# Kernel optimization log

Hardware: AMD Instinct MI355X
Metric: run time of the kernel (lower is better)

Reference implementation:

```python
import jax, jax.numpy as jnp
import numpy as np

N, E = 100000, 1600000
NODE_DIM, EDGE_DIM, HID = 128, 64, 128

def _mlp(x, w1, b1, w2, b2):
    # 2-layer MLP: Linear -> ReLU -> Linear (weights stored torch-style [out,in])
    return jax.nn.relu(x @ w1.T + b1) @ w2.T + b2

def setup_inputs() -> dict:
    key = jax.random.key(0)
    ks = jax.random.split(key, 24)
    g = lambda k, shp, fan: jax.random.normal(k, shp, jnp.float32) * (1.0 / np.sqrt(fan))
    return {
        "x": jax.random.normal(ks[0], (N, NODE_DIM), jnp.float32),
        "pos": jax.random.normal(ks[1], (N, 3), jnp.float32),
        "edge_index": jax.random.randint(ks[2], (2, E), 0, N),
        "edge_attr": jax.random.normal(ks[3], (E, EDGE_DIM), jnp.float32),
        # node_net: MLP(node_dim -> hid -> hid)
        "node_w1": g(ks[4], (HID, NODE_DIM), NODE_DIM), "node_b1": jnp.zeros((HID,), jnp.float32),
        "node_w2": g(ks[5], (HID, HID), HID), "node_b2": jnp.zeros((HID,), jnp.float32),
        # edge_net: MLP(edge_dim -> hid -> hid)
        "edge_w1": g(ks[6], (HID, EDGE_DIM), EDGE_DIM), "edge_b1": jnp.zeros((HID,), jnp.float32),
        "edge_w2": g(ks[7], (HID, HID), HID), "edge_b2": jnp.zeros((HID,), jnp.float32),
        # msg_net: Linear(hid, hid)
        "msg_w": g(ks[8], (HID, HID), HID), "msg_b": jnp.zeros((HID,), jnp.float32),
        # gate: MLP(edge_dim + node_dim -> hid -> hid)
        "gate_w1": g(ks[9], (HID, EDGE_DIM + NODE_DIM), EDGE_DIM + NODE_DIM), "gate_b1": jnp.zeros((HID,), jnp.float32),
        "gate_w2": g(ks[10], (HID, HID), HID), "gate_b2": jnp.zeros((HID,), jnp.float32),
        # centroid_lin: Linear(node_dim, hid)
        "cent_w": g(ks[11], (HID, NODE_DIM), NODE_DIM), "cent_b": jnp.zeros((HID,), jnp.float32),
        # layer norm
        "ln_g": jnp.ones((HID,), jnp.float32), "ln_b": jnp.zeros((HID,), jnp.float32),
        # out_transform: Linear(hid, node_dim)
        "out_w": g(ks[12], (NODE_DIM, HID), HID), "out_b": jnp.zeros((NODE_DIM,), jnp.float32),
    }

def reference(x, pos, edge_index, edge_attr,
              node_w1, node_b1, node_w2, node_b2,
              edge_w1, edge_b1, edge_w2, edge_b2,
              msg_w, msg_b,
              gate_w1, gate_b1, gate_w2, gate_b2,
              cent_w, cent_b, ln_g, ln_b, out_w, out_b):
    row, col = edge_index[0], edge_index[1]
    h_node = _mlp(x, node_w1, node_b1, node_w2, node_b2)          # (N, HID)
    h_edge = _mlp(edge_attr, edge_w1, edge_b1, edge_w2, edge_b2)   # (E, HID)
    msg_j = (h_edge * h_node[col]) @ msg_w.T + msg_b               # (E, HID)
    gate = _mlp(jnp.concatenate([edge_attr, x[col]], axis=-1),
                gate_w1, gate_b1, gate_w2, gate_b2)                # (E, HID)
    msg_j = msg_j * jax.nn.sigmoid(gate)
    aggr = jax.ops.segment_sum(msg_j, row, num_segments=x.shape[0])  # (N, HID)
    out = (x @ cent_w.T + cent_b) + aggr
    mu = jnp.mean(out, axis=-1, keepdims=True)
    var = jnp.var(out, axis=-1, keepdims=True)
    out = (out - mu) * jax.lax.rsqrt(var + 1e-5) * ln_g + ln_b
    return jax.nn.relu(out) @ out_w.T + out_b                      # (N, NODE_DIM)
```

## Files before the change

### kernel.cpp

```cpp
#include <hip/hip_runtime.h>

#define NN 100000
#define NE 1600000

typedef __bf16 bf16;
typedef bf16 bf16x8 __attribute__((ext_vector_type(8)));
typedef bf16 bf16x4 __attribute__((ext_vector_type(4)));
typedef float f32x4 __attribute__((ext_vector_type(4)));

__device__ __forceinline__ f32x4 mfma16(bf16x8 a, bf16x8 b, f32x4 c) {
    return __builtin_amdgcn_mfma_f32_16x16x32_bf16(a, b, c, 0, 0, 0);
}

__global__ void cvt_kernel(const float* __restrict__ s, bf16* __restrict__ d, int n4) {
    int i = blockIdx.x * 256 + threadIdx.x;
    if (i < n4) {
        f32x4 v = ((const f32x4*)s)[i];
        bf16x4 o;
        o[0] = (bf16)v[0]; o[1] = (bf16)v[1]; o[2] = (bf16)v[2]; o[3] = (bf16)v[3];
        ((bf16x4*)d)[i] = o;
    }
}

__launch_bounds__(256, 3)
__global__ void node_kernel(const bf16* __restrict__ xb,
                            const bf16* __restrict__ w1, const float* __restrict__ b1,
                            const bf16* __restrict__ w2, const float* __restrict__ b2,
                            const bf16* __restrict__ wc, const float* __restrict__ bc,
                            const bf16* __restrict__ wg1,
                            bf16* __restrict__ h_node, float* __restrict__ cent,
                            float* __restrict__ gx) {
    const int S = 136;
    __shared__ __align__(16) bf16 sX[64 * S];
    __shared__ __align__(16) bf16 sH[64 * S];
    const int tid = threadIdx.x;
    const int m0 = blockIdx.x * 64;
    {
        int e = tid >> 2, p = tid & 3;
        int gm = m0 + e;
        uint4 z = {0, 0, 0, 0};
        uint4* dst = (uint4*)(sX + e * S + p * 32);
        if (gm < NN) {
            const uint4* src = (const uint4*)(xb + (size_t)gm * 128 + p * 32);
#pragma unroll
            for (int j = 0; j < 4; ++j) dst[j] = src[j];
        } else {
#pragma unroll
            for (int j = 0; j < 4; ++j) dst[j] = z;
        }
    }
    __syncthreads();
    const int lane = tid & 63, wave = tid >> 6, t16 = lane & 15, quad = lane >> 4;
    const int n0 = wave * 32, koff = quad * 8;
    const f32x4 z4 = {0.f, 0.f, 0.f, 0.f};
    f32x4 acc[4][2];

#pragma unroll
    for (int mt = 0; mt < 4; ++mt) { acc[mt][0] = z4; acc[mt][1] = z4; }
#pragma unroll
    for (int ks = 0; ks < 4; ++ks) {
        bf16x8 bb0 = *(const bf16x8*)(w1 + (n0 + t16) * 128 + ks * 32 + koff);
        bf16x8 bb1 = *(const bf16x8*)(w1 + (n0 + 16 + t16) * 128 + ks * 32 + koff);
#pragma unroll
        for (int mt = 0; mt < 4; ++mt) {
            bf16x8 a = *(const bf16x8*)(sX + (mt * 16 + t16) * S + ks * 32 + koff);
            acc[mt][0] = mfma16(a, bb0, acc[mt][0]);
            acc[mt][1] = mfma16(a, bb1, acc[mt][1]);
        }
    }
    {
        float bi0 = b1[n0 + t16], bi1 = b1[n0 + 16 + t16];
#pragma unroll
        for (int mt = 0; mt < 4; ++mt)
#pragma unroll
            for (int nt = 0; nt < 2; ++nt) {
                int n = n0 + nt * 16 + t16;
                float bb = nt ? bi1 : bi0;
#pragma unroll
                for (int r = 0; r < 4; ++r) {
                    float v = acc[mt][nt][r] + bb;
                    sH[(mt * 16 + quad * 4 + r) * S + n] = (bf16)(v > 0.f ? v : 0.f);
                }
            }
    }
    __syncthreads();

#pragma unroll
    for (int mt = 0; mt < 4; ++mt) { acc[mt][0] = z4; acc[mt][1] = z4; }
#pragma unroll
    for (int ks = 0; ks < 4; ++ks) {
        bf16x8 bb0 = *(const bf16x8*)(w2 + (n0 + t16) * 128 + ks * 32 + koff);
        bf16x8 bb1 = *(const bf16x8*)(w2 + (n0 + 16 + t16) * 128 + ks * 32 + koff);
#pragma unroll
        for (int mt = 0; mt < 4; ++mt) {
            bf16x8 a = *(const bf16x8*)(sH + (mt * 16 + t16) * S + ks * 32 + koff);
            acc[mt][0] = mfma16(a, bb0, acc[mt][0]);
            acc[mt][1] = mfma16(a, bb1, acc[mt][1]);
        }
    }
    {
        float bi0 = b2[n0 + t16], bi1 = b2[n0 + 16 + t16];
#pragma unroll
        for (int mt = 0; mt < 4; ++mt)
#pragma unroll
            for (int nt = 0; nt < 2; ++nt) {
                int n = n0 + nt * 16 + t16;
                float bb = nt ? bi1 : bi0;
#pragma unroll
                for (int r = 0; r < 4; ++r) {
                    int gm = m0 + mt * 16 + quad * 4 + r;
                    if (gm < NN) h_node[(size_t)gm * 128 + n] = (bf16)(acc[mt][nt][r] + bb);
                }
            }
    }

#pragma unroll
    for (int mt = 0; mt < 4; ++mt) { acc[mt][0] = z4; acc[mt][1] = z4; }
#pragma unroll
    for (int ks = 0; ks < 4; ++ks) {
        bf16x8 bb0 = *(const bf16x8*)(wc + (n0 + t16) * 128 + ks * 32 + koff);
        bf16x8 bb1 = *(const bf16x8*)(wc + (n0 + 16 + t16) * 128 + ks * 32 + koff);
#pragma unroll
        for (int mt = 0; mt < 4; ++mt) {
            bf16x8 a = *(const bf16x8*)(sX + (mt * 16 + t16) * S + ks * 32 + koff);
            acc[mt][0] = mfma16(a, bb0, acc[mt][0]);
            acc[mt][1] = mfma16(a, bb1, acc[mt][1]);
        }
    }
    {
        float bi0 = bc[n0 + t16], bi1 = bc[n0 + 16 + t16];
#pragma unroll
        for (int mt = 0; mt < 4; ++mt)
#pragma unroll
            for (int nt = 0; nt < 2; ++nt) {
                int n = n0 + nt * 16 + t16;
                float bb = nt ? bi1 : bi0;
#pragma unroll
                for (int r = 0; r < 4; ++r) {
                    int gm = m0 + mt * 16 + quad * 4 + r;
                    if (gm < NN) cent[(size_t)gm * 128 + n] = acc[mt][nt][r] + bb;
                }
            }
    }

#pragma unroll
    for (int mt = 0; mt < 4; ++mt) { acc[mt][0] = z4; acc[mt][1] = z4; }
#pragma unroll
    for (int ks = 0; ks < 4; ++ks) {
        bf16x8 bb0 = *(const bf16x8*)(wg1 + (n0 + t16) * 192 + 64 + ks * 32 + koff);
        bf16x8 bb1 = *(const bf16x8*)(wg1 + (n0 + 16 + t16) * 192 + 64 + ks * 32 + koff);
#pragma unroll
        for (int mt = 0; mt < 4; ++mt) {
            bf16x8 a = *(const bf16x8*)(sX + (mt * 16 + t16) * S + ks * 32 + koff);
            acc[mt][0] = mfma16(a, bb0, acc[mt][0]);
            acc[mt][1] = mfma16(a, bb1, acc[mt][1]);
        }
    }
#pragma unroll
    for (int mt = 0; mt < 4; ++mt)
#pragma unroll
        for (int nt = 0; nt < 2; ++nt) {
            int n = n0 + nt * 16 + t16;
#pragma unroll
            for (int r = 0; r < 4; ++r) {
                int gm = m0 + mt * 16 + quad * 4 + r;
                if (gm < NN) gx[(size_t)gm * 128 + n] = acc[mt][nt][r];
            }
        }
}

__launch_bounds__(256, 3)
__global__ void edge_kernel(const float* __restrict__ edge_attr,
                            const int* __restrict__ erow, const int* __restrict__ ecol,
                            const bf16* __restrict__ hnode, const float* __restrict__ gx,
                            const bf16* __restrict__ we1, const float* __restrict__ be1,
                            const bf16* __restrict__ we2, const float* __restrict__ be2,
                            const bf16* __restrict__ wm, const float* __restrict__ bm,
                            const bf16* __restrict__ wg1, const float* __restrict__ bg1,
                            const bf16* __restrict__ wg2, const float* __restrict__ bg2,
                            float* __restrict__ aggr) {
    const int SE = 72, S = 136;
    __shared__ __align__(16) bf16 sEA[64 * SE];
    __shared__ __align__(16) bf16 sX[64 * S];
    __shared__ __align__(16) bf16 sT[64 * S];
    __shared__ int rowS[64], colS[64];
    const int tid = threadIdx.x;
    const int e0 = blockIdx.x * 64;
    if (tid < 64) { rowS[tid] = erow[e0 + tid]; colS[tid] = ecol[e0 + tid]; }
    __syncthreads();
#pragma unroll
    for (int i = 0; i < 4; ++i) {
        int idx = tid * 4 + i * 1024;
        int e = idx >> 6, k = idx & 63;
        f32x4 v = *(const f32x4*)(edge_attr + (size_t)(e0 + e) * 64 + k);
        bf16x4 o;
        o[0] = (bf16)v[0]; o[1] = (bf16)v[1]; o[2] = (bf16)v[2]; o[3] = (bf16)v[3];
        *(bf16x4*)(sEA + e * SE + k) = o;
    }
    {
        int e = tid >> 2, p = tid & 3;
        const uint4* src = (const uint4*)(hnode + (size_t)colS[e] * 128 + p * 32);
        uint4* dst = (uint4*)(sX + e * S + p * 32);
#pragma unroll
        for (int j = 0; j < 4; ++j) dst[j] = src[j];
    }
    __syncthreads();
    const int lane = tid & 63, wave = tid >> 6, t16 = lane & 15, quad = lane >> 4;
    const int n0 = wave * 32, koff = quad * 8;
    const f32x4 z4 = {0.f, 0.f, 0.f, 0.f};
    f32x4 acc[4][2];

    float gval[4][2][4];
#pragma unroll
    for (int mt = 0; mt < 4; ++mt)
#pragma unroll
        for (int r = 0; r < 4; ++r) {
            const float* grow = gx + (size_t)colS[mt * 16 + quad * 4 + r] * 128;
            gval[mt][0][r] = grow[n0 + t16];
            gval[mt][1][r] = grow[n0 + 16 + t16];
        }
#pragma unroll
    for (int mt = 0; mt < 4; ++mt) { acc[mt][0] = z4; acc[mt][1] = z4; }
#pragma unroll
    for (int ks = 0; ks < 2; ++ks) {
        bf16x8 bb0 = *(const bf16x8*)(wg1 + (n0 + t16) * 192 + ks * 32 + koff);
        bf16x8 bb1 = *(const bf16x8*)(wg1 + (n0 + 16 + t16) * 192 + ks * 32 + koff);
#pragma unroll
        for (int mt = 0; mt < 4; ++mt) {
            bf16x8 a = *(const bf16x8*)(sEA + (mt * 16 + t16) * SE + ks * 32 + koff);
            acc[mt][0] = mfma16(a, bb0, acc[mt][0]);
            acc[mt][1] = mfma16(a, bb1, acc[mt][1]);
        }
    }
    {
        float bi0 = bg1[n0 + t16], bi1 = bg1[n0 + 16 + t16];
#pragma unroll
        for (int mt = 0; mt < 4; ++mt)
#pragma unroll
            for (int nt = 0; nt < 2; ++nt) {
                int n = n0 + nt * 16 + t16;
                float bb = nt ? bi1 : bi0;
#pragma unroll
                for (int r = 0; r < 4; ++r) {
                    float v = acc[mt][nt][r] + bb + gval[mt][nt][r];
                    sT[(mt * 16 + quad * 4 + r) * S + n] = (bf16)(v > 0.f ? v : 0.f);
                }
            }
    }
    __syncthreads();

    f32x4 gsig[4][2];
#pragma unroll
    for (int mt = 0; mt < 4; ++mt) { gsig[mt][0] = z4; gsig[mt][1] = z4; acc[mt][0] = z4; acc[mt][1] = z4; }
#pragma unroll
    for (int ks = 0; ks < 4; ++ks) {
        bf16x8 bb0 = *(const bf16x8*)(wg2 + (n0 + t16) * 128 + ks * 32 + koff);
        bf16x8 bb1 = *(const bf16x8*)(wg2 + (n0 + 16 + t16) * 128 + ks * 32 + koff);
#pragma unroll
        for (int mt = 0; mt < 4; ++mt) {
            bf16x8 a = *(const bf16x8*)(sT + (mt * 16 + t16) * S + ks * 32 + koff);
            gsig[mt][0] = mfma16(a, bb0, gsig[mt][0]);
            gsig[mt][1] = mfma16(a, bb1, gsig[mt][1]);
        }
    }
#pragma unroll
    for (int ks = 0; ks < 2; ++ks) {
        bf16x8 bb0 = *(const bf16x8*)(we1 + (n0 + t16) * 64 + ks * 32 + koff);
        bf16x8 bb1 = *(const bf16x8*)(we1 + (n0 + 16 + t16) * 64 + ks * 32 + koff);
#pragma unroll
        for (int mt = 0; mt < 4; ++mt) {
            bf16x8 a = *(const bf16x8*)(sEA + (mt * 16 + t16) * SE + ks * 32 + koff);
            acc[mt][0] = mfma16(a, bb0, acc[mt][0]);
            acc[mt][1] = mfma16(a, bb1, acc[mt][1]);
        }
    }
    __syncthreads();
    {
        float bi0 = bg2[n0 + t16], bi1 = bg2[n0 + 16 + t16];
#pragma unroll
        for (int mt = 0; mt < 4; ++mt)
#pragma unroll
            for (int nt = 0; nt < 2; ++nt) {
                float bb = nt ? bi1 : bi0;
#pragma unroll
                for (int r = 0; r < 4; ++r) {
                    float v = gsig[mt][nt][r] + bb;
                    gsig[mt][nt][r] = 1.f / (1.f + __expf(-v));
                }
            }
    }
    {
        float bi0 = be1[n0 + t16], bi1 = be1[n0 + 16 + t16];
#pragma unroll
        for (int mt = 0; mt < 4; ++mt)
#pragma unroll
            for (int nt = 0; nt < 2; ++nt) {
                int n = n0 + nt * 16 + t16;
                float bb = nt ? bi1 : bi0;
#pragma unroll
                for (int r = 0; r < 4; ++r) {
                    float v = acc[mt][nt][r] + bb;
                    sT[(mt * 16 + quad * 4 + r) * S + n] = (bf16)(v > 0.f ? v : 0.f);
                }
            }
    }
    __syncthreads();

#pragma unroll
    for (int mt = 0; mt < 4; ++mt) { acc[mt][0] = z4; acc[mt][1] = z4; }
#pragma unroll
    for (int ks = 0; ks < 4; ++ks) {
        bf16x8 bb0 = *(const bf16x8*)(we2 + (n0 + t16) * 128 + ks * 32 + koff);
        bf16x8 bb1 = *(const bf16x8*)(we2 + (n0 + 16 + t16) * 128 + ks * 32 + koff);
#pragma unroll
        for (int mt = 0; mt < 4; ++mt) {
            bf16x8 a = *(const bf16x8*)(sT + (mt * 16 + t16) * S + ks * 32 + koff);
            acc[mt][0] = mfma16(a, bb0, acc[mt][0]);
            acc[mt][1] = mfma16(a, bb1, acc[mt][1]);
        }
    }
    {
        float bi0 = be2[n0 + t16], bi1 = be2[n0 + 16 + t16];
#pragma unroll
        for (int mt = 0; mt < 4; ++mt)
#pragma unroll
            for (int nt = 0; nt < 2; ++nt) {
                int n = n0 + nt * 16 + t16;
                float bb = nt ? bi1 : bi0;
#pragma unroll
                for (int r = 0; r < 4; ++r) {
                    float v = acc[mt][nt][r] + bb;
                    float hv = (float)sX[(mt * 16 + quad * 4 + r) * S + n];
                    acc[mt][nt][r] = v * hv;
                }
            }
    }
    __syncthreads();
#pragma unroll
    for (int mt = 0; mt < 4; ++mt)
#pragma unroll
        for (int nt = 0; nt < 2; ++nt) {
            int n = n0 + nt * 16 + t16;
#pragma unroll
            for (int r = 0; r < 4; ++r) {
                float p = acc[mt][nt][r];
                bf16 hi = (bf16)p;
                sT[(mt * 16 + quad * 4 + r) * S + n] = hi;
                sX[(mt * 16 + quad * 4 + r) * S + n] = (bf16)(p - (float)hi);
            }
        }
    __syncthreads();

#pragma unroll
    for (int mt = 0; mt < 4; ++mt) { acc[mt][0] = z4; acc[mt][1] = z4; }
#pragma unroll
    for (int ks = 0; ks < 4; ++ks) {
        bf16x8 bb0 = *(const bf16x8*)(wm + (n0 + t16) * 128 + ks * 32 + koff);
        bf16x8 bb1 = *(const bf16x8*)(wm + (n0 + 16 + t16) * 128 + ks * 32 + koff);
#pragma unroll
        for (int mt = 0; mt < 4; ++mt) {
            bf16x8 a = *(const bf16x8*)(sT + (mt * 16 + t16) * S + ks * 32 + koff);
            acc[mt][0] = mfma16(a, bb0, acc[mt][0]);
            acc[mt][1] = mfma16(a, bb1, acc[mt][1]);
        }
    }
#pragma unroll
    for (int ks = 0; ks < 4; ++ks) {
        bf16x8 bb0 = *(const bf16x8*)(wm + (n0 + t16) * 128 + ks * 32 + koff);
        bf16x8 bb1 = *(const bf16x8*)(wm + (n0 + 16 + t16) * 128 + ks * 32 + koff);
#pragma unroll
        for (int mt = 0; mt < 4; ++mt) {
            bf16x8 a = *(const bf16x8*)(sX + (mt * 16 + t16) * S + ks * 32 + koff);
            acc[mt][0] = mfma16(a, bb0, acc[mt][0]);
            acc[mt][1] = mfma16(a, bb1, acc[mt][1]);
        }
    }
    {
        float bi0 = bm[n0 + t16], bi1 = bm[n0 + 16 + t16];
#pragma unroll
        for (int mt = 0; mt < 4; ++mt)
#pragma unroll
            for (int nt = 0; nt < 2; ++nt) {
                int n = n0 + nt * 16 + t16;
                float bb = nt ? bi1 : bi0;
#pragma unroll
                for (int r = 0; r < 4; ++r) {
                    int mloc = mt * 16 + quad * 4 + r;
                    float v = (acc[mt][nt][r] + bb) * gsig[mt][nt][r];
                    atomicAdd(aggr + (size_t)rowS[mloc] * 128 + n, v);
                }
            }
    }
}

__launch_bounds__(256, 3)
__global__ void final_kernel(const float* __restrict__ cent, const float* __restrict__ aggr,
                             const float* __restrict__ lng, const float* __restrict__ lnb,
                             const bf16* __restrict__ wo, const float* __restrict__ bo,
                             float* __restrict__ out) {
    const int S = 136;
    __shared__ __align__(16) bf16 sA[128 * S];
    const int tid = threadIdx.x;
    const int m0 = blockIdx.x * 128;
    {
        int r = tid >> 1, h = tid & 1;
        int gm = m0 + r;
        f32x4 vb[16];
        float sum = 0.f, sq = 0.f;
        if (gm < NN) {
            const f32x4* c4 = (const f32x4*)(cent + (size_t)gm * 128 + h * 64);
            const f32x4* a4 = (const f32x4*)(aggr + (size_t)gm * 128 + h * 64);
#pragma unroll
            for (int j = 0; j < 16; ++j) {
                f32x4 v = c4[j] + a4[j];
                vb[j] = v;
                sum += v[0] + v[1] + v[2] + v[3];
                sq += v[0] * v[0] + v[1] * v[1] + v[2] * v[2] + v[3] * v[3];
            }
        } else {
            f32x4 z = {0.f, 0.f, 0.f, 0.f};
#pragma unroll
            for (int j = 0; j < 16; ++j) vb[j] = z;
        }
        sum += __shfl_xor(sum, 1);
        sq += __shfl_xor(sq, 1);
        float mu = sum * (1.f / 128.f);
        float var = sq * (1.f / 128.f) - mu * mu;
        float rs = rsqrtf(var + 1e-5f);
#pragma unroll
        for (int j = 0; j < 16; ++j) {
            bf16x4 o;
#pragma unroll
            for (int c = 0; c < 4; ++c) {
                int k = h * 64 + j * 4 + c;
                float y = (vb[j][c] - mu) * rs * lng[k] + lnb[k];
                y = y > 0.f ? y : 0.f;
                o[c] = (bf16)(gm < NN ? y : 0.f);
            }
            *(bf16x4*)(sA + r * S + h * 64 + j * 4) = o;
        }
    }
    __syncthreads();
    const int lane = tid & 63, wave = tid >> 6, t16 = lane & 15, quad = lane >> 4;
    const int n0 = wave * 32, koff = quad * 8;
    const f32x4 z4 = {0.f, 0.f, 0.f, 0.f};
    f32x4 acc[8][2];
#pragma unroll
    for (int mt = 0; mt < 8; ++mt) { acc[mt][0] = z4; acc[mt][1] = z4; }
#pragma unroll
    for (int ks = 0; ks < 4; ++ks) {
        bf16x8 bb0 = *(const bf16x8*)(wo + (n0 + t16) * 128 + ks * 32 + koff);
        bf16x8 bb1 = *(const bf16x8*)(wo + (n0 + 16 + t16) * 128 + ks * 32 + koff);
#pragma unroll
        for (int mt = 0; mt < 8; ++mt) {
            bf16x8 a = *(const bf16x8*)(sA + (mt * 16 + t16) * S + ks * 32 + koff);
            acc[mt][0] = mfma16(a, bb0, acc[mt][0]);
            acc[mt][1] = mfma16(a, bb1, acc[mt][1]);
        }
    }
    {
        float bi0 = bo[n0 + t16], bi1 = bo[n0 + 16 + t16];
#pragma unroll
        for (int mt = 0; mt < 8; ++mt)
#pragma unroll
            for (int nt = 0; nt < 2; ++nt) {
                int n = n0 + nt * 16 + t16;
                float bb = nt ? bi1 : bi0;
#pragma unroll
                for (int r = 0; r < 4; ++r) {
                    int gm = m0 + mt * 16 + quad * 4 + r;
                    if (gm < NN) out[(size_t)gm * 128 + n] = acc[mt][nt][r] + bb;
                }
            }
    }
}

extern "C" void kernel_launch(void* const* d_in, const int* in_sizes, int n_in,
                              void* d_out, int out_size, void* d_ws, size_t ws_size,
                              hipStream_t stream) {
    bf16* wsb = (bf16*)d_ws;
    bf16* nw1 = wsb + 0;
    bf16* nw2 = wsb + 16384;
    bf16* cw = wsb + 32768;
    bf16* ew1 = wsb + 49152;
    bf16* ew2 = wsb + 57344;
    bf16* mw = wsb + 73728;
    bf16* gw1 = wsb + 90112;
    bf16* gw2 = wsb + 114688;
    bf16* ow = wsb + 131072;
    bf16* xb = wsb + 147456;
    bf16* hb = xb + (size_t)NN * 128;
    float* cent = (float*)(hb + (size_t)NN * 128);
    float* aggr = cent + (size_t)NN * 128;
    float* gx = aggr + (size_t)NN * 128;

    auto cv = [&](int idx, bf16* dst, int n) {
        cvt_kernel<<<(n / 4 + 255) / 256, 256, 0, stream>>>((const float*)d_in[idx], dst, n / 4);
    };
    cv(4, nw1, 16384);
    cv(6, nw2, 16384);
    cv(18, cw, 16384);
    cv(8, ew1, 8192);
    cv(10, ew2, 16384);
    cv(12, mw, 16384);
    cv(14, gw1, 24576);
    cv(16, gw2, 16384);
    cv(22, ow, 16384);
    cv(0, xb, NN * 128);
    hipMemsetAsync(aggr, 0, (size_t)NN * 128 * sizeof(float), stream);

    node_kernel<<<(NN + 63) / 64, 256, 0, stream>>>(
        xb, nw1, (const float*)d_in[5], nw2, (const float*)d_in[7],
        cw, (const float*)d_in[19], gw1, hb, cent, gx);

    const int* ei = (const int*)d_in[2];
    edge_kernel<<<NE / 64, 256, 0, stream>>>(
        (const float*)d_in[3], ei, ei + NE, hb, gx,
        ew1, (const float*)d_in[9], ew2, (const float*)d_in[11],
        mw, (const float*)d_in[13], gw1, (const float*)d_in[15],
        gw2, (const float*)d_in[17], aggr);

    final_kernel<<<(NN + 127) / 128, 256, 0, stream>>>(
        cent, aggr, (const float*)d_in[20], (const float*)d_in[21],
        ow, (const float*)d_in[23], (float*)d_out);
}
```

Baseline: 1.402 ms.

## Restructure edge kernel so each wave owns 16 edges with all output columns

The edge kernel now gives each wave its own 16 edges and computes all 128 output columns per wave. Previously four waves split the columns of a shared 64-edge tile, which needed block-wide syncs, so this removes every __syncthreads and gives each wave private LDS tiles. h_node is now stored in fp32 and gathered straight into registers instead of staged in LDS as bf16, and s_setprio is raised around the MFMA loops. In exchange, weight fragments are reloaded per wave from global/L1 with less reuse across the 16-row tile, h_node gather traffic doubles, and register pressure rises.

```diff
diff --git a/kernel.cpp b/kernel.cpp
--- a/kernel.cpp
+++ b/kernel.cpp
@@ -28,7 +28,7 @@
                             const bf16* __restrict__ w2, const float* __restrict__ b2,
                             const bf16* __restrict__ wc, const float* __restrict__ bc,
                             const bf16* __restrict__ wg1,
-                            bf16* __restrict__ h_node, float* __restrict__ cent,
+                            float* __restrict__ h_node, float* __restrict__ cent,
                             float* __restrict__ gx) {
     const int S = 136;
     __shared__ __align__(16) bf16 sX[64 * S];
@@ -109,7 +109,7 @@
 #pragma unroll
                 for (int r = 0; r < 4; ++r) {
                     int gm = m0 + mt * 16 + quad * 4 + r;
-                    if (gm < NN) h_node[(size_t)gm * 128 + n] = (bf16)(acc[mt][nt][r] + bb);
+                    if (gm < NN) h_node[(size_t)gm * 128 + n] = acc[mt][nt][r] + bb;
                 }
             }
     }
@@ -172,7 +172,7 @@
 __launch_bounds__(256, 3)
 __global__ void edge_kernel(const float* __restrict__ edge_attr,
                             const int* __restrict__ erow, const int* __restrict__ ecol,
-                            const bf16* __restrict__ hnode, const float* __restrict__ gx,
+                            const float* __restrict__ hnode, const float* __restrict__ gx,
                             const bf16* __restrict__ we1, const float* __restrict__ be1,
                             const bf16* __restrict__ we2, const float* __restrict__ be2,
                             const bf16* __restrict__ wm, const float* __restrict__ bm,
@@ -180,216 +180,179 @@
                             const bf16* __restrict__ wg2, const float* __restrict__ bg2,
                             float* __restrict__ aggr) {
     const int SE = 72, S = 136;
-    __shared__ __align__(16) bf16 sEA[64 * SE];
-    __shared__ __align__(16) bf16 sX[64 * S];
-    __shared__ __align__(16) bf16 sT[64 * S];
-    __shared__ int rowS[64], colS[64];
+    __shared__ __align__(16) bf16 sEA[4][16 * SE];
+    __shared__ __align__(16) bf16 sT[4][16 * S];
+    __shared__ __align__(16) bf16 sL[4][16 * S];
     const int tid = threadIdx.x;
-    const int e0 = blockIdx.x * 64;
-    if (tid < 64) { rowS[tid] = erow[e0 + tid]; colS[tid] = ecol[e0 + tid]; }
-    __syncthreads();
-#pragma unroll
-    for (int i = 0; i < 4; ++i) {
-        int idx = tid * 4 + i * 1024;
-        int e = idx >> 6, k = idx & 63;
-        f32x4 v = *(const f32x4*)(edge_attr + (size_t)(e0 + e) * 64 + k);
-        bf16x4 o;
-        o[0] = (bf16)v[0]; o[1] = (bf16)v[1]; o[2] = (bf16)v[2]; o[3] = (bf16)v[3];
-        *(bf16x4*)(sEA + e * SE + k) = o;
-    }
-    {
-        int e = tid >> 2, p = tid & 3;
-        const uint4* src = (const uint4*)(hnode + (size_t)colS[e] * 128 + p * 32);
-        uint4* dst = (uint4*)(sX + e * S + p * 32);
-#pragma unroll
-        for (int j = 0; j < 4; ++j) dst[j] = src[j];
-    }
-    __syncthreads();
-    const int lane = tid & 63, wave = tid >> 6, t16 = lane & 15, quad = lane >> 4;
-    const int n0 = wave * 32, koff = quad * 8;
+    const int wave = tid >> 6, lane = tid & 63, t16 = lane & 15, quad = lane >> 4;
+    const int koff = quad * 8;
+    const int e0w = blockIdx.x * 64 + wave * 16;
+    bf16* sEAw = sEA[wave];
+    bf16* sTw = sT[wave];
+    bf16* sLw = sL[wave];
     const f32x4 z4 = {0.f, 0.f, 0.f, 0.f};
-    f32x4 acc[4][2];
-
-    float gval[4][2][4];
-#pragma unroll
-    for (int mt = 0; mt < 4; ++mt)
-#pragma unroll
-        for (int r = 0; r < 4; ++r) {
-            const float* grow = gx + (size_t)colS[mt * 16 + quad * 4 + r] * 128;
-            gval[mt][0][r] = grow[n0 + t16];
-            gval[mt][1][r] = grow[n0 + 16 + t16];
-        }
-#pragma unroll
-    for (int mt = 0; mt < 4; ++mt) { acc[mt][0] = z4; acc[mt][1] = z4; }
-#pragma unroll
-    for (int ks = 0; ks < 2; ++ks) {
-        bf16x8 bb0 = *(const bf16x8*)(wg1 + (n0 + t16) * 192 + ks * 32 + koff);
-        bf16x8 bb1 = *(const bf16x8*)(wg1 + (n0 + 16 + t16) * 192 + ks * 32 + koff);
-#pragma unroll
-        for (int mt = 0; mt < 4; ++mt) {
-            bf16x8 a = *(const bf16x8*)(sEA + (mt * 16 + t16) * SE + ks * 32 + koff);
-            acc[mt][0] = mfma16(a, bb0, acc[mt][0]);
-            acc[mt][1] = mfma16(a, bb1, acc[mt][1]);
-        }
-    }
-    {
-        float bi0 = bg1[n0 + t16], bi1 = bg1[n0 + 16 + t16];
-#pragma unroll
-        for (int mt = 0; mt < 4; ++mt)
-#pragma unroll
-            for (int nt = 0; nt < 2; ++nt) {
-                int n = n0 + nt * 16 + t16;
-                float bb = nt ? bi1 : bi0;
-#pragma unroll
-                for (int r = 0; r < 4; ++r) {
-                    float v = acc[mt][nt][r] + bb + gval[mt][nt][r];
-                    sT[(mt * 16 + quad * 4 + r) * S + n] = (bf16)(v > 0.f ? v : 0.f);
-                }
-            }
-    }
-    __syncthreads();
-
-    f32x4 gsig[4][2];
-#pragma unroll
-    for (int mt = 0; mt < 4; ++mt) { gsig[mt][0] = z4; gsig[mt][1] = z4; acc[mt][0] = z4; acc[mt][1] = z4; }
-#pragma unroll
-    for (int ks = 0; ks < 4; ++ks) {
-        bf16x8 bb0 = *(const bf16x8*)(wg2 + (n0 + t16) * 128 + ks * 32 + koff);
-        bf16x8 bb1 = *(const bf16x8*)(wg2 + (n0 + 16 + t16) * 128 + ks * 32 + koff);
-#pragma unroll
-        for (int mt = 0; mt < 4; ++mt) {
-            bf16x8 a = *(const bf16x8*)(sT + (mt * 16 + t16) * S + ks * 32 + koff);
-            gsig[mt][0] = mfma16(a, bb0, gsig[mt][0]);
-            gsig[mt][1] = mfma16(a, bb1, gsig[mt][1]);
-        }
-    }
-#pragma unroll
-    for (int ks = 0; ks < 2; ++ks) {
-        bf16x8 bb0 = *(const bf16x8*)(we1 + (n0 + t16) * 64 + ks * 32 + koff);
-        bf16x8 bb1 = *(const bf16x8*)(we1 + (n0 + 16 + t16) * 64 + ks * 32 + koff);
-#pragma unroll
-        for (int mt = 0; mt < 4; ++mt) {
-            bf16x8 a = *(const bf16x8*)(sEA + (mt * 16 + t16) * SE + ks * 32 + koff);
-            acc[mt][0] = mfma16(a, bb0, acc[mt][0]);
-            acc[mt][1] = mfma16(a, bb1, acc[mt][1]);
-        }
-    }
-    __syncthreads();
-    {
-        float bi0 = bg2[n0 + t16], bi1 = bg2[n0 + 16 + t16];
-#pragma unroll
-        for (int mt = 0; mt < 4; ++mt)
-#pragma unroll
-            for (int nt = 0; nt < 2; ++nt) {
-                float bb = nt ? bi1 : bi0;
-#pragma unroll
-                for (int r = 0; r < 4; ++r) {
-                    float v = gsig[mt][nt][r] + bb;
-                    gsig[mt][nt][r] = 1.f / (1.f + __expf(-v));
-                }
-            }
-    }
-    {
-        float bi0 = be1[n0 + t16], bi1 = be1[n0 + 16 + t16];
-#pragma unroll
-        for (int mt = 0; mt < 4; ++mt)
-#pragma unroll
-            for (int nt = 0; nt < 2; ++nt) {
-                int n = n0 + nt * 16 + t16;
-                float bb = nt ? bi1 : bi0;
-#pragma unroll
-                for (int r = 0; r < 4; ++r) {
-                    float v = acc[mt][nt][r] + bb;
-                    sT[(mt * 16 + quad * 4 + r) * S + n] = (bf16)(v > 0.f ? v : 0.f);
-                }
-            }
-    }
-    __syncthreads();
-
-#pragma unroll
-    for (int mt = 0; mt < 4; ++mt) { acc[mt][0] = z4; acc[mt][1] = z4; }
-#pragma unroll
-    for (int ks = 0; ks < 4; ++ks) {
-        bf16x8 bb0 = *(const bf16x8*)(we2 + (n0 + t16) * 128 + ks * 32 + koff);
-        bf16x8 bb1 = *(const bf16x8*)(we2 + (n0 + 16 + t16) * 128 + ks * 32 + koff);
-#pragma unroll
-        for (int mt = 0; mt < 4; ++mt) {
-            bf16x8 a = *(const bf16x8*)(sT + (mt * 16 + t16) * S + ks * 32 + koff);
-            acc[mt][0] = mfma16(a, bb0, acc[mt][0]);
-            acc[mt][1] = mfma16(a, bb1, acc[mt][1]);
-        }
-    }
-    {
-        float bi0 = be2[n0 + t16], bi1 = be2[n0 + 16 + t16];
-#pragma unroll
-        for (int mt = 0; mt < 4; ++mt)
-#pragma unroll
-            for (int nt = 0; nt < 2; ++nt) {
-                int n = n0 + nt * 16 + t16;
-                float bb = nt ? bi1 : bi0;
-#pragma unroll
-                for (int r = 0; r < 4; ++r) {
-                    float v = acc[mt][nt][r] + bb;
-                    float hv = (float)sX[(mt * 16 + quad * 4 + r) * S + n];
-                    acc[mt][nt][r] = v * hv;
-                }
-            }
-    }
-    __syncthreads();
-#pragma unroll
-    for (int mt = 0; mt < 4; ++mt)
-#pragma unroll
-        for (int nt = 0; nt < 2; ++nt) {
-            int n = n0 + nt * 16 + t16;
-#pragma unroll
-            for (int r = 0; r < 4; ++r) {
-                float p = acc[mt][nt][r];
+
+    int col4[4], rowA4[4];
+#pragma unroll
+    for (int r = 0; r < 4; ++r) {
+        col4[r] = ecol[e0w + quad * 4 + r];
+        rowA4[r] = erow[e0w + quad * 4 + r];
+    }
+
+    float gval[8][4];
+#pragma unroll
+    for (int r = 0; r < 4; ++r) {
+        const float* g = gx + (size_t)col4[r] * 128 + t16;
+#pragma unroll
+        for (int nt = 0; nt < 8; ++nt) gval[nt][r] = g[nt * 16];
+    }
+
+    {
+        int el = lane >> 2, q = lane & 3;
+        const f32x4* src = (const f32x4*)(edge_attr + (size_t)(e0w + el) * 64 + q * 16);
+        f32x4 v0 = src[0], v1 = src[1], v2 = src[2], v3 = src[3];
+        bf16x8 o0, o1;
+        o0[0] = (bf16)v0[0]; o0[1] = (bf16)v0[1]; o0[2] = (bf16)v0[2]; o0[3] = (bf16)v0[3];
+        o0[4] = (bf16)v1[0]; o0[5] = (bf16)v1[1]; o0[6] = (bf16)v1[2]; o0[7] = (bf16)v1[3];
+        o1[0] = (bf16)v2[0]; o1[1] = (bf16)v2[1]; o1[2] = (bf16)v2[2]; o1[3] = (bf16)v2[3];
+        o1[4] = (bf16)v3[0]; o1[5] = (bf16)v3[1]; o1[6] = (bf16)v3[2]; o1[7] = (bf16)v3[3];
+        *(bf16x8*)(sEAw + el * SE + q * 16) = o0;
+        *(bf16x8*)(sEAw + el * SE + q * 16 + 8) = o1;
+    }
+
+    {
+        f32x4 acc[8];
+#pragma unroll
+        for (int nt = 0; nt < 8; ++nt) acc[nt] = z4;
+        __builtin_amdgcn_s_setprio(1);
+#pragma unroll
+        for (int ks = 0; ks < 2; ++ks) {
+            bf16x8 a = *(const bf16x8*)(sEAw + t16 * SE + ks * 32 + koff);
+#pragma unroll
+            for (int nt = 0; nt < 8; ++nt) {
+                bf16x8 b = *(const bf16x8*)(wg1 + (nt * 16 + t16) * 192 + ks * 32 + koff);
+                acc[nt] = mfma16(a, b, acc[nt]);
+            }
+        }
+        __builtin_amdgcn_s_setprio(0);
+#pragma unroll
+        for (int nt = 0; nt < 8; ++nt) {
+            float bb = bg1[nt * 16 + t16];
+#pragma unroll
+            for (int r = 0; r < 4; ++r) {
+                float v = acc[nt][r] + bb + gval[nt][r];
+                sTw[(quad * 4 + r) * S + nt * 16 + t16] = (bf16)(v > 0.f ? v : 0.f);
+            }
+        }
+    }
+
+    float gsig[8][4];
+    {
+        f32x4 gacc[8], eacc[8];
+#pragma unroll
+        for (int nt = 0; nt < 8; ++nt) { gacc[nt] = z4; eacc[nt] = z4; }
+        __builtin_amdgcn_s_setprio(1);
+#pragma unroll
+        for (int ks = 0; ks < 4; ++ks) {
+            bf16x8 a = *(const bf16x8*)(sTw + t16 * S + ks * 32 + koff);
+#pragma unroll
+            for (int nt = 0; nt < 8; ++nt) {
+                bf16x8 b = *(const bf16x8*)(wg2 + (nt * 16 + t16) * 128 + ks * 32 + koff);
+                gacc[nt] = mfma16(a, b, gacc[nt]);
+            }
+        }
+#pragma unroll
+        for (int ks = 0; ks < 2; ++ks) {
+            bf16x8 a = *(const bf16x8*)(sEAw + t16 * SE + ks * 32 + koff);
+#pragma unroll
+            for (int nt = 0; nt < 8; ++nt) {
+                bf16x8 b = *(const bf16x8*)(we1 + (nt * 16 + t16) * 64 + ks * 32 + koff);
+                eacc[nt] = mfma16(a, b, eacc[nt]);
+            }
+        }
+        __builtin_amdgcn_s_setprio(0);
+#pragma unroll
+        for (int nt = 0; nt < 8; ++nt) {
+            float bb = bg2[nt * 16 + t16];
+#pragma unroll
+            for (int r = 0; r < 4; ++r) {
+                float v = gacc[nt][r] + bb;
+                gsig[nt][r] = 1.f / (1.f + __expf(-v));
+            }
+        }
+#pragma unroll
+        for (int nt = 0; nt < 8; ++nt) {
+            float bb = be1[nt * 16 + t16];
+#pragma unroll
+            for (int r = 0; r < 4; ++r) {
+                float v = eacc[nt][r] + bb;
+                sTw[(quad * 4 + r) * S + nt * 16 + t16] = (bf16)(v > 0.f ? v : 0.f);
+            }
+        }
+    }
+
+    float hval[8][4];
+#pragma unroll
+    for (int r = 0; r < 4; ++r) {
+        const float* h = hnode + (size_t)col4[r] * 128 + t16;
+#pragma unroll
+        for (int nt = 0; nt < 8; ++nt) hval[nt][r] = h[nt * 16];
+    }
+
+    {
+        f32x4 acc[8];
+#pragma unroll
+        for (int nt = 0; nt < 8; ++nt) acc[nt] = z4;
+        __builtin_amdgcn_s_setprio(1);
+#pragma unroll
+        for (int ks = 0; ks < 4; ++ks) {
+            bf16x8 a = *(const bf16x8*)(sTw + t16 * S + ks * 32 + koff);
+#pragma unroll
+            for (int nt = 0; nt < 8; ++nt) {
+                bf16x8 b = *(const bf16x8*)(we2 + (nt * 16 + t16) * 128 + ks * 32 + koff);
+                acc[nt] = mfma16(a, b, acc[nt]);
+            }
+        }
+        __builtin_amdgcn_s_setprio(0);
+#pragma unroll
+        for (int nt = 0; nt < 8; ++nt) {
+            float bb = be2[nt * 16 + t16];
+#pragma unroll
+            for (int r = 0; r < 4; ++r) {
+                float p = (acc[nt][r] + bb) * hval[nt][r];
                 bf16 hi = (bf16)p;
-                sT[(mt * 16 + quad * 4 + r) * S + n] = hi;
-                sX[(mt * 16 + quad * 4 + r) * S + n] = (bf16)(p - (float)hi);
-            }
-        }
-    __syncthreads();
-
-#pragma unroll
-    for (int mt = 0; mt < 4; ++mt) { acc[mt][0] = z4; acc[mt][1] = z4; }
-#pragma unroll
-    for (int ks = 0; ks < 4; ++ks) {
-        bf16x8 bb0 = *(const bf16x8*)(wm + (n0 + t16) * 128 + ks * 32 + koff);
-        bf16x8 bb1 = *(const bf16x8*)(wm + (n0 + 16 + t16) * 128 + ks * 32 + koff);
-#pragma unroll
-        for (int mt = 0; mt < 4; ++mt) {
-            bf16x8 a = *(const bf16x8*)(sT + (mt * 16 + t16) * S + ks * 32 + koff);
-            acc[mt][0] = mfma16(a, bb0, acc[mt][0]);
-            acc[mt][1] = mfma16(a, bb1, acc[mt][1]);
-        }
-    }
-#pragma unroll
-    for (int ks = 0; ks < 4; ++ks) {
-        bf16x8 bb0 = *(const bf16x8*)(wm + (n0 + t16) * 128 + ks * 32 + koff);
-        bf16x8 bb1 = *(const bf16x8*)(wm + (n0 + 16 + t16) * 128 + ks * 32 + koff);
-#pragma unroll
-        for (int mt = 0; mt < 4; ++mt) {
-            bf16x8 a = *(const bf16x8*)(sX + (mt * 16 + t16) * S + ks * 32 + koff);
-            acc[mt][0] = mfma16(a, bb0, acc[mt][0]);
-            acc[mt][1] = mfma16(a, bb1, acc[mt][1]);
-        }
-    }
-    {
-        float bi0 = bm[n0 + t16], bi1 = bm[n0 + 16 + t16];
-#pragma unroll
-        for (int mt = 0; mt < 4; ++mt)
-#pragma unroll
-            for (int nt = 0; nt < 2; ++nt) {
-                int n = n0 + nt * 16 + t16;
-                float bb = nt ? bi1 : bi0;
-#pragma unroll
-                for (int r = 0; r < 4; ++r) {
-                    int mloc = mt * 16 + quad * 4 + r;
-                    float v = (acc[mt][nt][r] + bb) * gsig[mt][nt][r];
-                    atomicAdd(aggr + (size_t)rowS[mloc] * 128 + n, v);
-                }
-            }
+                sTw[(quad * 4 + r) * S + nt * 16 + t16] = hi;
+                sLw[(quad * 4 + r) * S + nt * 16 + t16] = (bf16)(p - (float)hi);
+            }
+        }
+    }
+
+    {
+        f32x4 acc[8];
+#pragma unroll
+        for (int nt = 0; nt < 8; ++nt) acc[nt] = z4;
+        __builtin_amdgcn_s_setprio(1);
+#pragma unroll
+        for (int ks = 0; ks < 4; ++ks) {
+            bf16x8 ah = *(const bf16x8*)(sTw + t16 * S + ks * 32 + koff);
+            bf16x8 al = *(const bf16x8*)(sLw + t16 * S + ks * 32 + koff);
+#pragma unroll
+            for (int nt = 0; nt < 8; ++nt) {
+                bf16x8 b = *(const bf16x8*)(wm + (nt * 16 + t16) * 128 + ks * 32 + koff);
+                acc[nt] = mfma16(ah, b, acc[nt]);
+                acc[nt] = mfma16(al, b, acc[nt]);
+            }
+        }
+        __builtin_amdgcn_s_setprio(0);
+#pragma unroll
+        for (int nt = 0; nt < 8; ++nt) {
+            float bb = bm[nt * 16 + t16];
+#pragma unroll
+            for (int r = 0; r < 4; ++r) {
+                float v = (acc[nt][r] + bb) * gsig[nt][r];
+                atomicAdd(aggr + (size_t)rowA4[r] * 128 + nt * 16 + t16, v);
+            }
+        }
     }
 }
 
@@ -489,8 +452,8 @@
     bf16* gw2 = wsb + 114688;
     bf16* ow = wsb + 131072;
     bf16* xb = wsb + 147456;
-    bf16* hb = xb + (size_t)NN * 128;
-    float* cent = (float*)(hb + (size_t)NN * 128);
+    float* hb = (float*)(xb + (size_t)NN * 128);
+    float* cent = hb + (size_t)NN * 128;
     float* aggr = cent + (size_t)NN * 128;
     float* gx = aggr + (size_t)NN * 128;
 
```

Result: slower. 2.958 ms (+111.0%).

## Gather h_node as fp32 into registers instead of staging bf16 rows in LDS

Applied to the files above, without the earlier changes.

h_node is now stored in fp32, and the edge kernel gathers the needed h_node values straight into registers after the gate stage, rather than copying whole bf16 rows into shared memory up front. This frees one LDS buffer, which lets the buffers be reused in a different order and removes several __syncthreads barriers. The two split-precision message GEMM loops are also merged into one loop that shares the weight loads. The cost is twice the bytes per gathered h_node element, with scattered 4-byte global loads in place of 16-byte vector copies, plus an extra larger-footprint buffer in the workspace.

```diff
diff --git a/kernel.cpp b/kernel.cpp
--- a/kernel.cpp
+++ b/kernel.cpp
@@ -28,7 +28,7 @@
                             const bf16* __restrict__ w2, const float* __restrict__ b2,
                             const bf16* __restrict__ wc, const float* __restrict__ bc,
                             const bf16* __restrict__ wg1,
-                            bf16* __restrict__ h_node, float* __restrict__ cent,
+                            float* __restrict__ h_node, float* __restrict__ cent,
                             float* __restrict__ gx) {
     const int S = 136;
     __shared__ __align__(16) bf16 sX[64 * S];
@@ -109,7 +109,7 @@
 #pragma unroll
                 for (int r = 0; r < 4; ++r) {
                     int gm = m0 + mt * 16 + quad * 4 + r;
-                    if (gm < NN) h_node[(size_t)gm * 128 + n] = (bf16)(acc[mt][nt][r] + bb);
+                    if (gm < NN) h_node[(size_t)gm * 128 + n] = acc[mt][nt][r] + bb;
                 }
             }
     }
@@ -172,7 +172,7 @@
 __launch_bounds__(256, 3)
 __global__ void edge_kernel(const float* __restrict__ edge_attr,
                             const int* __restrict__ erow, const int* __restrict__ ecol,
-                            const bf16* __restrict__ hnode, const float* __restrict__ gx,
+                            const float* __restrict__ hnode, const float* __restrict__ gx,
                             const bf16* __restrict__ we1, const float* __restrict__ be1,
                             const bf16* __restrict__ we2, const float* __restrict__ be2,
                             const bf16* __restrict__ wm, const float* __restrict__ bm,
@@ -181,13 +181,12 @@
                             float* __restrict__ aggr) {
     const int SE = 72, S = 136;
     __shared__ __align__(16) bf16 sEA[64 * SE];
+    __shared__ __align__(16) bf16 sT[64 * S];
     __shared__ __align__(16) bf16 sX[64 * S];
-    __shared__ __align__(16) bf16 sT[64 * S];
     __shared__ int rowS[64], colS[64];
     const int tid = threadIdx.x;
     const int e0 = blockIdx.x * 64;
     if (tid < 64) { rowS[tid] = erow[e0 + tid]; colS[tid] = ecol[e0 + tid]; }
-    __syncthreads();
 #pragma unroll
     for (int i = 0; i < 4; ++i) {
         int idx = tid * 4 + i * 1024;
@@ -197,13 +196,6 @@
         o[0] = (bf16)v[0]; o[1] = (bf16)v[1]; o[2] = (bf16)v[2]; o[3] = (bf16)v[3];
         *(bf16x4*)(sEA + e * SE + k) = o;
     }
-    {
-        int e = tid >> 2, p = tid & 3;
-        const uint4* src = (const uint4*)(hnode + (size_t)colS[e] * 128 + p * 32);
-        uint4* dst = (uint4*)(sX + e * S + p * 32);
-#pragma unroll
-        for (int j = 0; j < 4; ++j) dst[j] = src[j];
-    }
     __syncthreads();
     const int lane = tid & 63, wave = tid >> 6, t16 = lane & 15, quad = lane >> 4;
     const int n0 = wave * 32, koff = quad * 8;
@@ -219,6 +211,7 @@
             gval[mt][0][r] = grow[n0 + t16];
             gval[mt][1][r] = grow[n0 + 16 + t16];
         }
+
 #pragma unroll
     for (int mt = 0; mt < 4; ++mt) { acc[mt][0] = z4; acc[mt][1] = z4; }
 #pragma unroll
@@ -274,7 +267,6 @@
             acc[mt][1] = mfma16(a, bb1, acc[mt][1]);
         }
     }
-    __syncthreads();
     {
         float bi0 = bg2[n0 + t16], bi1 = bg2[n0 + 16 + t16];
 #pragma unroll
@@ -300,11 +292,21 @@
 #pragma unroll
                 for (int r = 0; r < 4; ++r) {
                     float v = acc[mt][nt][r] + bb;
-                    sT[(mt * 16 + quad * 4 + r) * S + n] = (bf16)(v > 0.f ? v : 0.f);
-                }
-            }
-    }
-    __syncthreads();
+                    sX[(mt * 16 + quad * 4 + r) * S + n] = (bf16)(v > 0.f ? v : 0.f);
+                }
+            }
+    }
+    __syncthreads();
+
+    float hval[4][2][4];
+#pragma unroll
+    for (int mt = 0; mt < 4; ++mt)
+#pragma unroll
+        for (int r = 0; r < 4; ++r) {
+            const float* h = hnode + (size_t)colS[mt * 16 + quad * 4 + r] * 128;
+            hval[mt][0][r] = h[n0 + t16];
+            hval[mt][1][r] = h[n0 + 16 + t16];
+        }
 
 #pragma unroll
     for (int mt = 0; mt < 4; ++mt) { acc[mt][0] = z4; acc[mt][1] = z4; }
@@ -314,7 +316,7 @@
         bf16x8 bb1 = *(const bf16x8*)(we2 + (n0 + 16 + t16) * 128 + ks * 32 + koff);
 #pragma unroll
         for (int mt = 0; mt < 4; ++mt) {
-            bf16x8 a = *(const bf16x8*)(sT + (mt * 16 + t16) * S + ks * 32 + koff);
+            bf16x8 a = *(const bf16x8*)(sX + (mt * 16 + t16) * S + ks * 32 + koff);
             acc[mt][0] = mfma16(a, bb0, acc[mt][0]);
             acc[mt][1] = mfma16(a, bb1, acc[mt][1]);
         }
@@ -325,17 +327,14 @@
         for (int mt = 0; mt < 4; ++mt)
 #pragma unroll
             for (int nt = 0; nt < 2; ++nt) {
-                int n = n0 + nt * 16 + t16;
-                float bb = nt ? bi1 : bi0;
-#pragma unroll
-                for (int r = 0; r < 4; ++r) {
-                    float v = acc[mt][nt][r] + bb;
-                    float hv = (float)sX[(mt * 16 + quad * 4 + r) * S + n];
-                    acc[mt][nt][r] = v * hv;
-                }
-            }
-    }
-    __syncthreads();
+                float bb = nt ? bi1 : bi0;
+#pragma unroll
+                for (int r = 0; r < 4; ++r)
+                    acc[mt][nt][r] = (acc[mt][nt][r] + bb) * hval[mt][nt][r];
+            }
+    }
+    __syncthreads();
+
 #pragma unroll
     for (int mt = 0; mt < 4; ++mt)
 #pragma unroll
@@ -359,20 +358,12 @@
         bf16x8 bb1 = *(const bf16x8*)(wm + (n0 + 16 + t16) * 128 + ks * 32 + koff);
 #pragma unroll
         for (int mt = 0; mt < 4; ++mt) {
-            bf16x8 a = *(const bf16x8*)(sT + (mt * 16 + t16) * S + ks * 32 + koff);
-            acc[mt][0] = mfma16(a, bb0, acc[mt][0]);
-            acc[mt][1] = mfma16(a, bb1, acc[mt][1]);
-        }
-    }
-#pragma unroll
-    for (int ks = 0; ks < 4; ++ks) {
-        bf16x8 bb0 = *(const bf16x8*)(wm + (n0 + t16) * 128 + ks * 32 + koff);
-        bf16x8 bb1 = *(const bf16x8*)(wm + (n0 + 16 + t16) * 128 + ks * 32 + koff);
-#pragma unroll
-        for (int mt = 0; mt < 4; ++mt) {
-            bf16x8 a = *(const bf16x8*)(sX + (mt * 16 + t16) * S + ks * 32 + koff);
-            acc[mt][0] = mfma16(a, bb0, acc[mt][0]);
-            acc[mt][1] = mfma16(a, bb1, acc[mt][1]);
+            bf16x8 ah = *(const bf16x8*)(sT + (mt * 16 + t16) * S + ks * 32 + koff);
+            bf16x8 al = *(const bf16x8*)(sX + (mt * 16 + t16) * S + ks * 32 + koff);
+            acc[mt][0] = mfma16(ah, bb0, acc[mt][0]);
+            acc[mt][0] = mfma16(al, bb0, acc[mt][0]);
+            acc[mt][1] = mfma16(ah, bb1, acc[mt][1]);
+            acc[mt][1] = mfma16(al, bb1, acc[mt][1]);
         }
     }
     {
@@ -489,8 +480,8 @@
     bf16* gw2 = wsb + 114688;
     bf16* ow = wsb + 131072;
     bf16* xb = wsb + 147456;
-    bf16* hb = xb + (size_t)NN * 128;
-    float* cent = (float*)(hb + (size_t)NN * 128);
+    float* hb = (float*)(xb + (size_t)NN * 128);
+    float* cent = hb + (size_t)NN * 128;
     float* aggr = cent + (size_t)NN * 128;
     float* gx = aggr + (size_t)NN * 128;
 
```

After: 1.419 ms. About the same (+1.3%).
